# Optimization experiments

Hardware: AMD Instinct MI355X
Metric: run time of the kernel (lower is better)

## Reference

```python
import jax, jax.numpy as jnp
import numpy as np

B, NB, K, C, CM, POS = 8, 1024, 9, 32, 128, 2
SIGMA = 0.5
NEG_SLOPE = 0.01  # nn.LeakyReLU default
BN_EPS = 1e-5


def _leaky(x):
    return jnp.where(x >= 0, x, NEG_SLOPE * x)


def _batchnorm(x, gamma, beta):
    # BatchNorm1d, training-mode batch statistics over the point dimension
    mu = jnp.mean(x, axis=0)
    var = jnp.mean((x - mu) ** 2, axis=0)
    return gamma * (x - mu) * jax.lax.rsqrt(var + BN_EPS) + beta


def setup_inputs() -> dict:
    key = jax.random.key(0)
    ks = jax.random.split(key, 8)
    N = B * NB
    positions = jax.random.normal(ks[0], (N, POS), jnp.float32)
    weights = jax.random.normal(ks[1], (N, C), jnp.float32)
    batch = jnp.full((B,), NB, dtype=jnp.int32)  # uniform point counts per graph
    # KernelConv params: kernel_init='grid' -> 3x3 grid of offsets spanning +-sigma
    g = jnp.linspace(-SIGMA, SIGMA, 3, dtype=jnp.float32)
    kernel_positions = jnp.stack(jnp.meshgrid(g, g, indexing='ij'), axis=-1).reshape(K, POS)
    kernel_weights = (jax.random.normal(ks[2], (K, C, C), jnp.float32) / np.float32(np.sqrt(C * K)))
    conv_norm_gamma = jnp.ones((C,), jnp.float32)
    conv_norm_beta = jnp.zeros((C,), jnp.float32)
    # PyG MLP([C, CM, C+POS], act_first=True, plain_last=True)
    W1 = jax.random.normal(ks[3], (C, CM), jnp.float32) / np.float32(np.sqrt(C))
    b1 = jnp.zeros((CM,), jnp.float32)
    bn_gamma = jnp.ones((CM,), jnp.float32)
    bn_beta = jnp.zeros((CM,), jnp.float32)
    W2 = jax.random.normal(ks[4], (CM, C + POS), jnp.float32) / np.float32(np.sqrt(CM))
    b2 = jnp.zeros((C + POS,), jnp.float32)
    return dict(positions=positions, weights=weights, batch=batch,
                kernel_positions=kernel_positions, kernel_weights=kernel_weights,
                conv_norm_gamma=conv_norm_gamma, conv_norm_beta=conv_norm_beta,
                W1=W1, b1=b1, bn_gamma=bn_gamma, bn_beta=bn_beta, W2=W2, b2=b2)


def reference(positions, weights, batch, kernel_positions, kernel_weights,
              conv_norm_gamma, conv_norm_beta, W1, b1, bn_gamma, bn_beta, W2, b2):
    N = positions.shape[0]
    # --- KernelConv: each point spawns K components at pos + kernel offset ---
    conv_pos = (positions[:, None, :] + kernel_positions[None, :, :])  # [N,K,2]
    conv_w = jnp.einsum('nc,kcd->nkd', weights, kernel_weights)        # [N,K,C]
    conv_pos = conv_pos.reshape(B, NB * K, POS)
    conv_w = conv_w.reshape(B, NB * K, C)
    # --- KernelSample: evaluate Gaussian mixture at original positions ---
    p = positions.reshape(B, NB, POS)
    d2 = (jnp.sum(p * p, -1)[:, :, None]
          + jnp.sum(conv_pos * conv_pos, -1)[:, None, :]
          - 2.0 * jnp.einsum('bnd,bmd->bnm', p, conv_pos))             # [B,NB,NB*K]
    Kmat = jnp.exp(-d2 / (2.0 * SIGMA * SIGMA))
    sampled = jnp.einsum('bnm,bmc->bnc', Kmat, conv_w).reshape(N, C)
    x = _leaky(sampled)                                                 # KernelSample nonlinearity
    # conv_norm + residual add of input weights
    x = _batchnorm(x, conv_norm_gamma, conv_norm_beta) + weights
    # MLP: lin -> act -> batchnorm (act_first) -> plain last lin
    h = _batchnorm(_leaky(x @ W1 + b1), bn_gamma, bn_beta)
    mlp_out = h @ W2 + b2                                               # [N, POS + C]
    delta_pos, delta_w = mlp_out[:, :POS], mlp_out[:, POS:]
    return positions + delta_pos, x + delta_w
```

## Files before the change

kernel.cpp:

```cpp
#include <hip/hip_runtime.h>
#include <hip/hip_bf16.h>

#define BB    8
#define NBB   1024
#define KK    9
#define CC    32
#define CMM   128
#define NTOT  (BB*NBB)
#define MM    (NBB*KK)
#define NEG   0.01f
#define EPS   1e-5f
#define L2C   (-2.8853900817779268f)

#define OFF_CWT   0
#define SZ_CWT    (BB*CC*MM/2)
#define OFF_CFX   (OFF_CWT + SZ_CWT)
#define OFF_CFY   (OFF_CFX + BB*MM)
#define OFF_CF0   (OFF_CFY + BB*MM)
#define OFF_X0    (OFF_CF0 + BB*MM)
#define OFF_X     (OFF_X0 + NTOT*CC)
#define OFF_H0    (OFF_X + NTOT*CC)
#define OFF_ST    (OFF_H0 + NTOT*CMM)

typedef __attribute__((ext_vector_type(8))) short short8;
typedef __attribute__((ext_vector_type(4))) float f32x4;
typedef __attribute__((ext_vector_type(2))) float f32x2;

static __device__ __forceinline__ unsigned short f2bf_rne(float f) {
    __hip_bfloat16 h = __float2bfloat16(f);
    return *reinterpret_cast<unsigned short*>(&h);
}

__global__ __launch_bounds__(256) void k_convw(const float* __restrict__ pos,
                                               const float* __restrict__ kpos,
                                               const float* __restrict__ w,
                                               const float* __restrict__ kw,
                                               float* __restrict__ cfx,
                                               float* __restrict__ cfy,
                                               float* __restrict__ cf0,
                                               float* __restrict__ stats,
                                               short* __restrict__ cwT) {
    __shared__ unsigned short kwl[KK*CC*CC];
    __shared__ unsigned short tile[2*32*144];
    int t = threadIdx.x;
    int l = t & 63, wv = t >> 6;
    int lane15 = l & 15, quad = l >> 4;
    int blk = blockIdx.x;
    int b = blk & 7, nbl = blk >> 3;

    if (blk == 0 && t < 320) stats[t] = 0.f;
    #pragma unroll
    for (int rep = 0; rep < 2; ++rep) {
        int gid = rep*65536 + blk*256 + t;
        if (gid < BB*MM) {
            int bb = gid / MM;
            int m = gid - bb*MM;
            int np = m / 9, k9 = m - np*9;
            float qx = pos[((size_t)(bb*NBB + np))*2 + 0] + kpos[k9*2 + 0];
            float qy = pos[((size_t)(bb*NBB + np))*2 + 1] + kpos[k9*2 + 1];
            cfx[gid] = -2.f*L2C*qx;
            cfy[gid] = -2.f*L2C*qy;
            cf0[gid] = L2C*(qx*qx + qy*qy);
        }
    }
    for (int u = t; u < KK*CC*CC/4; u += 256) {
        int flat = u*4;
        int row = flat >> 5;
        int c0 = flat & 31;
        int kk = row >> 5, cp = row & 31;
        f32x4 v = *(const f32x4*)&kw[flat];
        kwl[(kk*CC + c0+0)*CC + cp] = f2bf_rne(v.x);
        kwl[(kk*CC + c0+1)*CC + cp] = f2bf_rne(v.y);
        kwl[(kk*CC + c0+2)*CC + cp] = f2bf_rne(v.z);
        kwl[(kk*CC + c0+3)*CC + cp] = f2bf_rne(v.w);
    }
    int n = b*NBB + nbl*32 + (wv & 1)*16 + lane15;
    f32x4 w0 = *(const f32x4*)&w[(size_t)n*CC + quad*8];
    f32x4 w1 = *(const f32x4*)&w[(size_t)n*CC + quad*8 + 4];
    union { unsigned short us[8]; short8 s; } bfr;
    bfr.us[0] = f2bf_rne(w0.x); bfr.us[1] = f2bf_rne(w0.y);
    bfr.us[2] = f2bf_rne(w0.z); bfr.us[3] = f2bf_rne(w0.w);
    bfr.us[4] = f2bf_rne(w1.x); bfr.us[5] = f2bf_rne(w1.y);
    bfr.us[6] = f2bf_rne(w1.z); bfr.us[7] = f2bf_rne(w1.w);
    __syncthreads();
    if (wv < 2) {
        f32x4 acc[KK][2];
        #pragma unroll
        for (int kk = 0; kk < KK; ++kk)
            #pragma unroll
            for (int ct = 0; ct < 2; ++ct) {
                int c = ct*16 + lane15;
                short8 afr = *(const short8*)&kwl[(kk*CC + c)*CC + quad*8];
                acc[kk][ct] = __builtin_amdgcn_mfma_f32_16x16x32_bf16(
                    afr, bfr.s, (f32x4)0.f, 0, 0, 0);
            }
        unsigned short* tw = tile + wv*4608;
        #pragma unroll
        for (int kk = 0; kk < KK; ++kk)
            #pragma unroll
            for (int ct = 0; ct < 2; ++ct)
                #pragma unroll
                for (int reg = 0; reg < 4; ++reg) {
                    int c = ct*16 + quad*4 + reg;
                    tw[c*144 + lane15*9 + kk] = f2bf_rne(acc[kk][ct][reg]);
                }
    }
    __syncthreads();
    short* dst = cwT + (size_t)b*CC*MM + (size_t)(nbl*32)*9;
    #pragma unroll
    for (int it = 0; it < 5; ++it) {
        int u = it*256 + t;
        if (u < 1152) {
            int c = u / 36, seg = u - c*36;
            const unsigned short* src = tile + (seg < 18 ? 0 : 4608)
                                      + c*144 + (seg < 18 ? seg : seg - 18)*8;
            short8 v = *(const short8*)src;
            *(short8*)&dst[(size_t)c*MM + seg*8] = v;
        }
    }
}

__global__ __launch_bounds__(1024) void k_sample(const float* __restrict__ pos,
                                                 const float* __restrict__ cfx,
                                                 const float* __restrict__ cfy,
                                                 const float* __restrict__ cf0,
                                                 const short* __restrict__ cwT,
                                                 float* __restrict__ x0,
                                                 float* __restrict__ s1) {
    __shared__ float red[16*32*36];
    __shared__ float sstat[64];
    int t = threadIdx.x;
    int l = t & 63, wv = t >> 6;
    int blk = blockIdx.x;
    int b = blk & 7, nblk = blk >> 3;
    int lane15 = l & 15, quad = l >> 4;
    int nbase = b*NBB + nblk*32;
    if (t < 64) sstat[t] = 0.f;

    float px[2], py[2], cn[2];
    #pragma unroll
    for (int nt = 0; nt < 2; ++nt) {
        int n = nbase + nt*16 + lane15;
        float x = pos[(size_t)n*2], y = pos[(size_t)n*2 + 1];
        px[nt] = x; py[nt] = y; cn[nt] = L2C*(x*x + y*y);
    }
    f32x4 acc[2][2];
    acc[0][0] = (f32x4)0.f; acc[0][1] = (f32x4)0.f;
    acc[1][0] = (f32x4)0.f; acc[1][1] = (f32x4)0.f;

    const float* bx = cfx + (size_t)b*MM;
    const float* by = cfy + (size_t)b*MM;
    const float* b0 = cf0 + (size_t)b*MM;
    const short* ca0 = cwT + (size_t)b*CC*MM + (size_t)lane15*MM;
    const short* ca1 = ca0 + (size_t)16*MM;

    int m0 = wv*576 + quad*8;
    #pragma unroll 2
    for (int kk = 0; kk < 18; ++kk, m0 += 32) {
        short8 a0 = *(const short8*)&ca0[m0];
        short8 a1 = *(const short8*)&ca1[m0];
        f32x4 vx0 = *(const f32x4*)&bx[m0];
        f32x4 vx1 = *(const f32x4*)&bx[m0 + 4];
        f32x4 vy0 = *(const f32x4*)&by[m0];
        f32x4 vy1 = *(const f32x4*)&by[m0 + 4];
        f32x4 v00 = *(const f32x4*)&b0[m0];
        f32x4 v01 = *(const f32x4*)&b0[m0 + 4];
        #pragma unroll
        for (int nt = 0; nt < 2; ++nt) {
            f32x2 Xv = {px[nt], px[nt]};
            f32x2 Yv = {py[nt], py[nt]};
            f32x2 Cv = {cn[nt], cn[nt]};
            f32x2 t0 = (f32x2){v00.x, v00.y} + Cv;
            t0 = (f32x2){vy0.x, vy0.y}*Yv + t0;
            t0 = (f32x2){vx0.x, vx0.y}*Xv + t0;
            f32x2 t1 = (f32x2){v00.z, v00.w} + Cv;
            t1 = (f32x2){vy0.z, vy0.w}*Yv + t1;
            t1 = (f32x2){vx0.z, vx0.w}*Xv + t1;
            f32x2 t2 = (f32x2){v01.x, v01.y} + Cv;
            t2 = (f32x2){vy1.x, vy1.y}*Yv + t2;
            t2 = (f32x2){vx1.x, vx1.y}*Xv + t2;
            f32x2 t3 = (f32x2){v01.z, v01.w} + Cv;
            t3 = (f32x2){vy1.z, vy1.w}*Yv + t3;
            t3 = (f32x2){vx1.z, vx1.w}*Xv + t3;
            float e0 = __builtin_amdgcn_exp2f(t0.x);
            float e1 = __builtin_amdgcn_exp2f(t0.y);
            float e2 = __builtin_amdgcn_exp2f(t1.x);
            float e3 = __builtin_amdgcn_exp2f(t1.y);
            float e4 = __builtin_amdgcn_exp2f(t2.x);
            float e5 = __builtin_amdgcn_exp2f(t2.y);
            float e6 = __builtin_amdgcn_exp2f(t3.x);
            float e7 = __builtin_amdgcn_exp2f(t3.y);
            union { unsigned int u[4]; short8 s; } bf;
            bf.u[0] = (__float_as_uint(e0) >> 16) | (__float_as_uint(e1) & 0xffff0000u);
            bf.u[1] = (__float_as_uint(e2) >> 16) | (__float_as_uint(e3) & 0xffff0000u);
            bf.u[2] = (__float_as_uint(e4) >> 16) | (__float_as_uint(e5) & 0xffff0000u);
            bf.u[3] = (__float_as_uint(e6) >> 16) | (__float_as_uint(e7) & 0xffff0000u);
            acc[nt][0] = __builtin_amdgcn_mfma_f32_16x16x32_bf16(a0, bf.s, acc[nt][0], 0, 0, 0);
            acc[nt][1] = __builtin_amdgcn_mfma_f32_16x16x32_bf16(a1, bf.s, acc[nt][1], 0, 0, 0);
        }
    }
    #pragma unroll
    for (int nt = 0; nt < 2; ++nt)
        #pragma unroll
        for (int ct = 0; ct < 2; ++ct) {
            int n = nt*16 + lane15, c = ct*16 + quad*4;
            *(f32x4*)&red[(wv*32 + n)*36 + c] = acc[nt][ct];
        }
    __syncthreads();
    if (t < 256) {
        int nr = t >> 3, c0 = (t & 7)*4;
        f32x4 v = (f32x4)0.f;
        #pragma unroll
        for (int wp = 0; wp < 16; ++wp)
            v = v + *(const f32x4*)&red[(wp*32 + nr)*36 + c0];
        v.x = v.x >= 0.f ? v.x : NEG*v.x;
        v.y = v.y >= 0.f ? v.y : NEG*v.y;
        v.z = v.z >= 0.f ? v.z : NEG*v.z;
        v.w = v.w >= 0.f ? v.w : NEG*v.w;
        *(f32x4*)&x0[((size_t)(nbase + nr))*CC + c0] = v;
        float s0 = v.x, s1v = v.y, s2v = v.z, s3v = v.w;
        float q0 = v.x*v.x, q1 = v.y*v.y, q2 = v.z*v.z, q3 = v.w*v.w;
        #pragma unroll
        for (int mk = 8; mk <= 32; mk <<= 1) {
            s0 += __shfl_xor(s0, mk); s1v += __shfl_xor(s1v, mk);
            s2v += __shfl_xor(s2v, mk); s3v += __shfl_xor(s3v, mk);
            q0 += __shfl_xor(q0, mk); q1 += __shfl_xor(q1, mk);
            q2 += __shfl_xor(q2, mk); q3 += __shfl_xor(q3, mk);
        }
        if (l < 8) {
            atomicAdd(&sstat[c0 + 0], s0);  atomicAdd(&sstat[c0 + 1], s1v);
            atomicAdd(&sstat[c0 + 2], s2v); atomicAdd(&sstat[c0 + 3], s3v);
            atomicAdd(&sstat[32 + c0 + 0], q0); atomicAdd(&sstat[32 + c0 + 1], q1);
            atomicAdd(&sstat[32 + c0 + 2], q2); atomicAdd(&sstat[32 + c0 + 3], q3);
        }
    }
    __syncthreads();
    if (t < 64) atomicAdd(&s1[t], sstat[t]);
}

__global__ __launch_bounds__(256) void k_mlp1(const float* __restrict__ x0,
                                              const float* __restrict__ wts,
                                              const float* __restrict__ gma,
                                              const float* __restrict__ bta,
                                              const float* __restrict__ W1,
                                              const float* __restrict__ b1,
                                              const float* __restrict__ s1,
                                              float* __restrict__ x,
                                              float* __restrict__ h0,
                                              float* __restrict__ s2) {
    __shared__ float tile[32*68];
    int t = threadIdx.x;
    int l = t & 63, wv = t >> 6;
    int blk = blockIdx.x;
    int nb = blk >> 2, jq = blk & 3;
    int n = nb*64 + l;
    int j0 = jq*32 + wv*8;

    float xv[32];
    #pragma unroll
    for (int c = 0; c < 32; ++c) {
        float mu  = s1[c] * (1.f/NTOT);
        float var = s1[32+c]*(1.f/NTOT) - mu*mu;
        float a   = gma[c] * rsqrtf(var + EPS);
        float v   = x0[(size_t)n*CC + c];
        xv[c] = a*(v - mu) + bta[c] + wts[(size_t)n*CC + c];
    }
    if (jq == 0 && wv == 0) {
        #pragma unroll
        for (int c = 0; c < 32; c += 4)
            *(float4*)&x[(size_t)n*CC + c] = make_float4(xv[c], xv[c+1], xv[c+2], xv[c+3]);
    }
    float acc[8];
    *(f32x4*)&acc[0] = *(const f32x4*)&b1[j0];
    *(f32x4*)&acc[4] = *(const f32x4*)&b1[j0 + 4];
    #pragma unroll 8
    for (int c = 0; c < 32; ++c) {
        float xc = xv[c];
        const float* w1r = W1 + c*CMM + j0;
        f32x4 wa = *(const f32x4*)&w1r[0];
        f32x4 wb = *(const f32x4*)&w1r[4];
        acc[0] = fmaf(xc, wa.x, acc[0]); acc[1] = fmaf(xc, wa.y, acc[1]);
        acc[2] = fmaf(xc, wa.z, acc[2]); acc[3] = fmaf(xc, wa.w, acc[3]);
        acc[4] = fmaf(xc, wb.x, acc[4]); acc[5] = fmaf(xc, wb.y, acc[5]);
        acc[6] = fmaf(xc, wb.z, acc[6]); acc[7] = fmaf(xc, wb.w, acc[7]);
    }
    #pragma unroll
    for (int jj = 0; jj < 8; ++jj) {
        acc[jj] = acc[jj] >= 0.f ? acc[jj] : NEG*acc[jj];
        tile[(wv*8 + jj)*68 + l] = acc[jj];
    }
    float* hd = h0 + (size_t)n*CMM + j0;
    *(float4*)&hd[0] = make_float4(acc[0], acc[1], acc[2], acc[3]);
    *(float4*)&hd[4] = make_float4(acc[4], acc[5], acc[6], acc[7]);
    __syncthreads();
    if (t < 256) {
        int jl = t >> 3, grp = t & 7;
        float lsum = 0.f, lsq = 0.f;
        #pragma unroll
        for (int q = 0; q < 2; ++q) {
            f32x4 v = *(const f32x4*)&tile[jl*68 + grp*8 + q*4];
            lsum += v.x + v.y + v.z + v.w;
            lsq = fmaf(v.x, v.x, fmaf(v.y, v.y, fmaf(v.z, v.z, fmaf(v.w, v.w, lsq))));
        }
        lsum += __shfl_xor(lsum, 1); lsq += __shfl_xor(lsq, 1);
        lsum += __shfl_xor(lsum, 2); lsq += __shfl_xor(lsq, 2);
        lsum += __shfl_xor(lsum, 4); lsq += __shfl_xor(lsq, 4);
        if (grp == 0) {
            int jg = jq*32 + jl;
            atomicAdd(&s2[jg], lsum);
            atomicAdd(&s2[CMM + jg], lsq);
        }
    }
}

__global__ __launch_bounds__(256) void k_mlp2(const float* __restrict__ h0,
                                              const float* __restrict__ x,
                                              const float* __restrict__ pos,
                                              const float* __restrict__ g2,
                                              const float* __restrict__ bt2,
                                              const float* __restrict__ W2,
                                              const float* __restrict__ b2,
                                              const float* __restrict__ s2,
                                              float* __restrict__ out) {
    __shared__ float red[16*16*35];
    int t = threadIdx.x;
    int nl = t & 15, rid = t >> 4;
    int n = blockIdx.x*16 + nl;
    int j0 = rid*8;
    float hv[8];
    *(f32x4*)&hv[0] = *(const f32x4*)&h0[(size_t)n*CMM + j0];
    *(f32x4*)&hv[4] = *(const f32x4*)&h0[(size_t)n*CMM + j0 + 4];
    #pragma unroll
    for (int jj = 0; jj < 8; ++jj) {
        int j = j0 + jj;
        float mu  = s2[j] * (1.f/NTOT);
        float var = s2[CMM+j]*(1.f/NTOT) - mu*mu;
        float a   = g2[j] * rsqrtf(var + EPS);
        hv[jj] = a*(hv[jj] - mu) + bt2[j];
    }
    float acc[34];
    #pragma unroll
    for (int c = 0; c < 34; ++c) acc[c] = 0.f;
    for (int jj = 0; jj < 8; ++jj) {
        float h = hv[jj];
        const float* w2r = W2 + (size_t)(j0 + jj)*34;
        #pragma unroll
        for (int c = 0; c < 34; ++c)
            acc[c] = fmaf(h, w2r[c], acc[c]);
    }
    #pragma unroll
    for (int c = 0; c < 34; ++c) red[(rid*16 + nl)*35 + c] = acc[c];
    __syncthreads();
    #pragma unroll
    for (int it = 0; it < 3; ++it) {
        int u = it*256 + t;
        if (u < 544) {
            int r = u / 34, c = u - r*34;
            float v = b2[c];
            #pragma unroll
            for (int rr = 0; rr < 16; ++rr) v += red[(rr*16 + r)*35 + c];
            int nn = blockIdx.x*16 + r;
            if (c < 2)
                out[(size_t)nn*2 + c] = pos[(size_t)nn*2 + c] + v;
            else
                out[16384 + (size_t)nn*32 + (c-2)] = x[(size_t)nn*32 + (c-2)] + v;
        }
    }
}

extern "C" void kernel_launch(void* const* d_in, const int* in_sizes, int n_in,
                              void* d_out, int out_size, void* d_ws, size_t ws_size,
                              hipStream_t stream) {
    const float* positions = (const float*)d_in[0];
    const float* weights   = (const float*)d_in[1];
    const float* kpos = (const float*)d_in[3];
    const float* kw   = (const float*)d_in[4];
    const float* cg   = (const float*)d_in[5];
    const float* cb   = (const float*)d_in[6];
    const float* W1   = (const float*)d_in[7];
    const float* b1   = (const float*)d_in[8];
    const float* bg   = (const float*)d_in[9];
    const float* bb   = (const float*)d_in[10];
    const float* W2   = (const float*)d_in[11];
    const float* b2   = (const float*)d_in[12];
    float* ws  = (float*)d_ws;
    float* out = (float*)d_out;

    float* s1 = ws + OFF_ST;
    float* s2 = ws + OFF_ST + 64;

    k_convw<<<256, 256, 0, stream>>>(positions, kpos, weights, kw,
                                     ws + OFF_CFX, ws + OFF_CFY, ws + OFF_CF0,
                                     s1, (short*)(ws + OFF_CWT));
    k_sample<<<256, 1024, 0, stream>>>(positions, ws + OFF_CFX, ws + OFF_CFY,
                                       ws + OFF_CF0, (const short*)(ws + OFF_CWT),
                                       ws + OFF_X0, s1);
    k_mlp1<<<512, 256, 0, stream>>>(ws + OFF_X0, weights, cg, cb, W1, b1,
                                    s1, ws + OFF_X, ws + OFF_H0, s2);
    k_mlp2<<<512, 256, 0, stream>>>(ws + OFF_H0, ws + OFF_X, positions,
                                    bg, bb, W2, b2, s2, out);
}
```

Before: 154.1 us.

## Compute Gaussian distance directly from scaled positions and software-pipeline sample loads

Replaces the expanded-quadratic distance form (three precomputed coefficient arrays) with direct difference-of-scaled-positions, so only two coordinate arrays are stored and read. The scaling by sqrt(log2 e / (2 sigma^2)) folds the exponent constant into the positions. The sample loop now prefetches the next iteration's operands into registers before computing the current one. This cuts global traffic by a third and hides load latency, at the cost of more live registers and dropping the unroll-2 pragma.

After: 149.1 us. 3.3% less time.

```diff
diff --git a/kernel.cpp b/kernel.cpp
--- a/kernel.cpp
+++ b/kernel.cpp
@@ -10,14 +10,13 @@
 #define MM    (NBB*KK)
 #define NEG   0.01f
 #define EPS   1e-5f
-#define L2C   (-2.8853900817779268f)
+#define SQL2  1.6986436f
 
 #define OFF_CWT   0
 #define SZ_CWT    (BB*CC*MM/2)
-#define OFF_CFX   (OFF_CWT + SZ_CWT)
-#define OFF_CFY   (OFF_CFX + BB*MM)
-#define OFF_CF0   (OFF_CFY + BB*MM)
-#define OFF_X0    (OFF_CF0 + BB*MM)
+#define OFF_QPX   (OFF_CWT + SZ_CWT)
+#define OFF_QPY   (OFF_QPX + BB*MM)
+#define OFF_X0    (OFF_QPY + BB*MM)
 #define OFF_X     (OFF_X0 + NTOT*CC)
 #define OFF_H0    (OFF_X + NTOT*CC)
 #define OFF_ST    (OFF_H0 + NTOT*CMM)
@@ -35,9 +34,8 @@
                                                const float* __restrict__ kpos,
                                                const float* __restrict__ w,
                                                const float* __restrict__ kw,
-                                               float* __restrict__ cfx,
-                                               float* __restrict__ cfy,
-                                               float* __restrict__ cf0,
+                                               float* __restrict__ qpx,
+                                               float* __restrict__ qpy,
                                                float* __restrict__ stats,
                                                short* __restrict__ cwT) {
     __shared__ unsigned short kwl[KK*CC*CC];
@@ -58,9 +56,8 @@
             int np = m / 9, k9 = m - np*9;
             float qx = pos[((size_t)(bb*NBB + np))*2 + 0] + kpos[k9*2 + 0];
             float qy = pos[((size_t)(bb*NBB + np))*2 + 1] + kpos[k9*2 + 1];
-            cfx[gid] = -2.f*L2C*qx;
-            cfy[gid] = -2.f*L2C*qy;
-            cf0[gid] = L2C*(qx*qx + qy*qy);
+            qpx[gid] = SQL2*qx;
+            qpy[gid] = SQL2*qy;
         }
     }
     for (int u = t; u < KK*CC*CC/4; u += 256) {
@@ -121,9 +118,8 @@
 }
 
 __global__ __launch_bounds__(1024) void k_sample(const float* __restrict__ pos,
-                                                 const float* __restrict__ cfx,
-                                                 const float* __restrict__ cfy,
-                                                 const float* __restrict__ cf0,
+                                                 const float* __restrict__ qpx,
+                                                 const float* __restrict__ qpy,
                                                  const short* __restrict__ cwT,
                                                  float* __restrict__ x0,
                                                  float* __restrict__ s1) {
@@ -137,59 +133,57 @@
     int nbase = b*NBB + nblk*32;
     if (t < 64) sstat[t] = 0.f;
 
-    float px[2], py[2], cn[2];
+    float px[2], py[2];
     #pragma unroll
     for (int nt = 0; nt < 2; ++nt) {
         int n = nbase + nt*16 + lane15;
-        float x = pos[(size_t)n*2], y = pos[(size_t)n*2 + 1];
-        px[nt] = x; py[nt] = y; cn[nt] = L2C*(x*x + y*y);
+        px[nt] = SQL2*pos[(size_t)n*2];
+        py[nt] = SQL2*pos[(size_t)n*2 + 1];
     }
     f32x4 acc[2][2];
     acc[0][0] = (f32x4)0.f; acc[0][1] = (f32x4)0.f;
     acc[1][0] = (f32x4)0.f; acc[1][1] = (f32x4)0.f;
 
-    const float* bx = cfx + (size_t)b*MM;
-    const float* by = cfy + (size_t)b*MM;
-    const float* b0 = cf0 + (size_t)b*MM;
+    const float* qx = qpx + (size_t)b*MM;
+    const float* qy = qpy + (size_t)b*MM;
     const short* ca0 = cwT + (size_t)b*CC*MM + (size_t)lane15*MM;
     const short* ca1 = ca0 + (size_t)16*MM;
 
     int m0 = wv*576 + quad*8;
-    #pragma unroll 2
-    for (int kk = 0; kk < 18; ++kk, m0 += 32) {
-        short8 a0 = *(const short8*)&ca0[m0];
-        short8 a1 = *(const short8*)&ca1[m0];
-        f32x4 vx0 = *(const f32x4*)&bx[m0];
-        f32x4 vx1 = *(const f32x4*)&bx[m0 + 4];
-        f32x4 vy0 = *(const f32x4*)&by[m0];
-        f32x4 vy1 = *(const f32x4*)&by[m0 + 4];
-        f32x4 v00 = *(const f32x4*)&b0[m0];
-        f32x4 v01 = *(const f32x4*)&b0[m0 + 4];
+    short8 a0 = *(const short8*)&ca0[m0];
+    short8 a1 = *(const short8*)&ca1[m0];
+    f32x4 X0 = *(const f32x4*)&qx[m0], X1 = *(const f32x4*)&qx[m0 + 4];
+    f32x4 Y0 = *(const f32x4*)&qy[m0], Y1 = *(const f32x4*)&qy[m0 + 4];
+    for (int kk = 0; kk < 18; ++kk) {
+        int mn = m0 + (kk < 17 ? 32 : 0);
+        short8 na0 = *(const short8*)&ca0[mn];
+        short8 na1 = *(const short8*)&ca1[mn];
+        f32x4 nX0 = *(const f32x4*)&qx[mn], nX1 = *(const f32x4*)&qx[mn + 4];
+        f32x4 nY0 = *(const f32x4*)&qy[mn], nY1 = *(const f32x4*)&qy[mn + 4];
         #pragma unroll
         for (int nt = 0; nt < 2; ++nt) {
-            f32x2 Xv = {px[nt], px[nt]};
-            f32x2 Yv = {py[nt], py[nt]};
-            f32x2 Cv = {cn[nt], cn[nt]};
-            f32x2 t0 = (f32x2){v00.x, v00.y} + Cv;
-            t0 = (f32x2){vy0.x, vy0.y}*Yv + t0;
-            t0 = (f32x2){vx0.x, vx0.y}*Xv + t0;
-            f32x2 t1 = (f32x2){v00.z, v00.w} + Cv;
-            t1 = (f32x2){vy0.z, vy0.w}*Yv + t1;
-            t1 = (f32x2){vx0.z, vx0.w}*Xv + t1;
-            f32x2 t2 = (f32x2){v01.x, v01.y} + Cv;
-            t2 = (f32x2){vy1.x, vy1.y}*Yv + t2;
-            t2 = (f32x2){vx1.x, vx1.y}*Xv + t2;
-            f32x2 t3 = (f32x2){v01.z, v01.w} + Cv;
-            t3 = (f32x2){vy1.z, vy1.w}*Yv + t3;
-            t3 = (f32x2){vx1.z, vx1.w}*Xv + t3;
-            float e0 = __builtin_amdgcn_exp2f(t0.x);
-            float e1 = __builtin_amdgcn_exp2f(t0.y);
-            float e2 = __builtin_amdgcn_exp2f(t1.x);
-            float e3 = __builtin_amdgcn_exp2f(t1.y);
-            float e4 = __builtin_amdgcn_exp2f(t2.x);
-            float e5 = __builtin_amdgcn_exp2f(t2.y);
-            float e6 = __builtin_amdgcn_exp2f(t3.x);
-            float e7 = __builtin_amdgcn_exp2f(t3.y);
+            f32x2 PX = {px[nt], px[nt]};
+            f32x2 PY = {py[nt], py[nt]};
+            f32x2 dx0 = (f32x2){X0.x, X0.y} - PX;
+            f32x2 dy0 = (f32x2){Y0.x, Y0.y} - PY;
+            f32x2 t0 = dx0*dx0; t0 = dy0*dy0 + t0;
+            f32x2 dx1 = (f32x2){X0.z, X0.w} - PX;
+            f32x2 dy1 = (f32x2){Y0.z, Y0.w} - PY;
+            f32x2 t1 = dx1*dx1; t1 = dy1*dy1 + t1;
+            f32x2 dx2 = (f32x2){X1.x, X1.y} - PX;
+            f32x2 dy2 = (f32x2){Y1.x, Y1.y} - PY;
+            f32x2 t2 = dx2*dx2; t2 = dy2*dy2 + t2;
+            f32x2 dx3 = (f32x2){X1.z, X1.w} - PX;
+            f32x2 dy3 = (f32x2){Y1.z, Y1.w} - PY;
+            f32x2 t3 = dx3*dx3; t3 = dy3*dy3 + t3;
+            float e0 = __builtin_amdgcn_exp2f(-t0.x);
+            float e1 = __builtin_amdgcn_exp2f(-t0.y);
+            float e2 = __builtin_amdgcn_exp2f(-t1.x);
+            float e3 = __builtin_amdgcn_exp2f(-t1.y);
+            float e4 = __builtin_amdgcn_exp2f(-t2.x);
+            float e5 = __builtin_amdgcn_exp2f(-t2.y);
+            float e6 = __builtin_amdgcn_exp2f(-t3.x);
+            float e7 = __builtin_amdgcn_exp2f(-t3.y);
             union { unsigned int u[4]; short8 s; } bf;
             bf.u[0] = (__float_as_uint(e0) >> 16) | (__float_as_uint(e1) & 0xffff0000u);
             bf.u[1] = (__float_as_uint(e2) >> 16) | (__float_as_uint(e3) & 0xffff0000u);
@@ -198,6 +192,9 @@
             acc[nt][0] = __builtin_amdgcn_mfma_f32_16x16x32_bf16(a0, bf.s, acc[nt][0], 0, 0, 0);
             acc[nt][1] = __builtin_amdgcn_mfma_f32_16x16x32_bf16(a1, bf.s, acc[nt][1], 0, 0, 0);
         }
+        a0 = na0; a1 = na1;
+        X0 = nX0; X1 = nX1; Y0 = nY0; Y1 = nY1;
+        m0 = mn;
     }
     #pragma unroll
     for (int nt = 0; nt < 2; ++nt)
@@ -390,10 +387,10 @@
     float* s2 = ws + OFF_ST + 64;
 
     k_convw<<<256, 256, 0, stream>>>(positions, kpos, weights, kw,
-                                     ws + OFF_CFX, ws + OFF_CFY, ws + OFF_CF0,
+                                     ws + OFF_QPX, ws + OFF_QPY,
                                      s1, (short*)(ws + OFF_CWT));
-    k_sample<<<256, 1024, 0, stream>>>(positions, ws + OFF_CFX, ws + OFF_CFY,
-                                       ws + OFF_CF0, (const short*)(ws + OFF_CWT),
+    k_sample<<<256, 1024, 0, stream>>>(positions, ws + OFF_QPX, ws + OFF_QPY,
+                                       (const short*)(ws + OFF_CWT),
                                        ws + OFF_X0, s1);
     k_mlp1<<<512, 256, 0, stream>>>(ws + OFF_X0, weights, cg, cb, W1, b1,
                                     s1, ws + OFF_X, ws + OFF_H0, s2);
```
